# Performance work log

Measured on AMD Instinct MI355X. Metric: run time of the kernel, lower is better.

Reference implementation:

```python
import jax, jax.numpy as jnp
import numpy as np

H = 16
D_NOPE = 128
D_ROPE = 64
D_V = 128
ROPE_BASE = 10000.0
NEG = -1e9


def rotate_half(x):
    h = x.shape[-1] // 2
    return jnp.concatenate([-x[..., h:], x[..., :h]], axis=-1)


def rope_cos_sin(L, dtype=jnp.float32):
    inv_freq = 1.0 / (ROPE_BASE ** (jnp.arange(0, D_ROPE, 2, dtype=jnp.float32) / D_ROPE))
    t = jnp.arange(L, dtype=jnp.float32)
    freqs = jnp.outer(t, inv_freq)                      # (L, D_ROPE/2)
    emb = jnp.concatenate([freqs, freqs], axis=-1)      # (L, D_ROPE)
    return jnp.cos(emb)[None, None].astype(dtype), jnp.sin(emb)[None, None].astype(dtype)


def setup_inputs() -> dict:
    key = jax.random.key(0)
    ks = jax.random.split(key, 8)
    B, L, D = 1, 2048, 2048
    dq, dc = 1536, 512
    dqk = D_NOPE + D_ROPE
    s = 0.02
    hidden_states = jax.random.normal(ks[0], (B, L, D), jnp.float32)
    # causal additive mask, shape (B,1,L,L)
    causal = jnp.tril(jnp.ones((L, L), jnp.bool_))
    attention_mask = jnp.where(causal, 0.0, NEG).astype(jnp.float32)[None, None]
    return {
        "hidden_states": hidden_states,
        "attention_mask": attention_mask,
        "Wq_down": jax.random.normal(ks[1], (D, dq), jnp.float32) * s,
        "Wq_up": jax.random.normal(ks[2], (dq, H * dqk), jnp.float32) * s,
        "Wkv_down": jax.random.normal(ks[3], (D, dc), jnp.float32) * s,
        "Wk_up": jax.random.normal(ks[4], (dc, H * dqk), jnp.float32) * s,
        "Wv_up": jax.random.normal(ks[5], (dc, H * D_V), jnp.float32) * s,
        "Wo": jax.random.normal(ks[6], (H * D_V, D), jnp.float32) * s,
    }


def reference(hidden_states, attention_mask, Wq_down, Wq_up, Wkv_down, Wk_up, Wv_up, Wo):
    B, L, D = hidden_states.shape
    dqk = D_NOPE + D_ROPE
    scale = 1.0 / np.sqrt(dqk).astype(np.float32)

    # low-rank Q path
    q = (hidden_states @ Wq_down) @ Wq_up                       # (B,L,H*dqk)
    q = q.reshape(B, L, H, dqk).transpose(0, 2, 1, 3)           # (B,H,L,dqk)
    # low-rank KV path
    c_kv = hidden_states @ Wkv_down                             # (B,L,dc)
    k = (c_kv @ Wk_up).reshape(B, L, H, dqk).transpose(0, 2, 1, 3)
    v = (c_kv @ Wv_up).reshape(B, L, H, D_V).transpose(0, 2, 1, 3)

    q_nope, q_rope = q[..., :D_NOPE], q[..., D_NOPE:]
    k_nope, k_rope = k[..., :D_NOPE], k[..., D_NOPE:]
    cos, sin = rope_cos_sin(L, hidden_states.dtype)
    q_rope = q_rope * cos + rotate_half(q_rope) * sin
    k_rope = k_rope * cos + rotate_half(k_rope) * sin
    q = jnp.concatenate([q_nope, q_rope], axis=-1)
    k = jnp.concatenate([k_nope, k_rope], axis=-1)

    scores = jnp.einsum("bhqd,bhkd->bhqk", q, k) * scale + attention_mask
    weights = jax.nn.softmax(scores.astype(jnp.float32), axis=-1).astype(q.dtype)
    attn = jnp.einsum("bhqk,bhkd->bhqd", weights, v)            # (B,H,L,D_V)
    attn = attn.transpose(0, 2, 1, 3).reshape(B, L, H * D_V)
    return attn @ Wo
```

## Files before the change

kernel.cpp:

```cpp
#include <hip/hip_runtime.h>
#include <hip/hip_bf16.h>

using bf16 = __hip_bfloat16;
typedef __bf16 bf16x8v __attribute__((ext_vector_type(8)));
typedef float f32x4 __attribute__((ext_vector_type(4)));

static constexpr int SEQ = 2048;
static constexpr int DMODEL = 2048;
static constexpr int NHEADS = 16;
static constexpr int DQKC = 192;
static constexpr int DVC = 128;
static constexpr int DQC = 1536;
static constexpr int DCC = 512;
static constexpr int HQK = NHEADS * DQKC;
static constexpr int HV = NHEADS * DVC;
static constexpr int NKV = HQK + HV;
static constexpr int NDOWN = DQC + DCC;

typedef __attribute__((address_space(1))) const void* gas_ptr;
typedef __attribute__((address_space(3))) void* las_ptr;

__device__ __forceinline__ void g2l16(const void* g, void* l) {
  __builtin_amdgcn_global_load_lds((gas_ptr)g, (las_ptr)l, 16, 0, 0);
}

template <int BM, int BN>
__device__ __forceinline__ void gemm_core(
    const bf16* __restrict__ A, int lda,
    const bf16* __restrict__ Bt, int ldb,
    void* __restrict__ Cv, int ldc,
    int K, float alpha, int c_fp32, long tm, long tn, char* smem)
{
  constexpr int FM = BM / 32, FN = BN / 32;
  bf16* As = (bf16*)smem;
  char* Bsm = smem + BM * 64;
  bf16* Bs = (bf16*)Bsm;
  const int tid = threadIdx.x;
  const int w = tid >> 6, lane = tid & 63;
  const int wm = (w >> 1) * (BM / 2), wn = (w & 1) * (BN / 2);
  const int m0 = lane & 15, q8 = (lane >> 4) * 8;
  f32x4 acc[FM][FN] = {};
  for (int bk = 0; bk < K; bk += 32) {
#pragma unroll
    for (int i = 0; i < BM / 64; i++) {
      const int u = i * 256 + tid;
      g2l16(A + (tm + (u >> 2)) * (long)lda + bk + (u & 3) * 8, smem + u * 16);
    }
#pragma unroll
    for (int i = 0; i < BN / 64; i++) {
      const int u = i * 256 + tid;
      g2l16(Bt + (tn + (u >> 2)) * (long)ldb + bk + (u & 3) * 8, Bsm + u * 16);
    }
    __syncthreads();
    bf16x8v af[FM], bfv[FN];
#pragma unroll
    for (int i = 0; i < FM; i++)
      af[i] = *reinterpret_cast<const bf16x8v*>(&As[(wm + i * 16 + m0) * 32 + q8]);
#pragma unroll
    for (int i = 0; i < FN; i++)
      bfv[i] = *reinterpret_cast<const bf16x8v*>(&Bs[(wn + i * 16 + m0) * 32 + q8]);
#pragma unroll
    for (int mi = 0; mi < FM; mi++)
#pragma unroll
      for (int ni = 0; ni < FN; ni++)
        acc[mi][ni] = __builtin_amdgcn_mfma_f32_16x16x32_bf16(af[mi], bfv[ni], acc[mi][ni], 0, 0, 0);
    __syncthreads();
  }
  const int q4 = (lane >> 4) * 4;
  float* Cf = (float*)Cv;
  bf16* Cb = (bf16*)Cv;
#pragma unroll
  for (int mi = 0; mi < FM; mi++) {
#pragma unroll
    for (int r = 0; r < 4; r++) {
      const long row = tm + wm + mi * 16 + q4 + r;
#pragma unroll
      for (int ni = 0; ni < FN; ni++) {
        const long idx = row * ldc + tn + wn + ni * 16 + m0;
        const float v = acc[mi][ni][r] * alpha;
        if (c_fp32) Cf[idx] = v;
        else Cb[idx] = __float2bfloat16(v);
      }
    }
  }
}

__global__ __launch_bounds__(256) void gemm64(
    const bf16* __restrict__ A, int lda, const bf16* __restrict__ Bt, int ldb,
    void* __restrict__ Cv, int ldc, int K, float alpha, int c_fp32)
{
  __shared__ __align__(16) char smem[(64 + 128) * 64];
  gemm_core<64, 128>(A, lda, Bt, ldb, Cv, ldc, K, alpha, c_fp32,
                     (long)blockIdx.y * 64, (long)blockIdx.x * 128, smem);
}

__global__ __launch_bounds__(256) void gemm_dual(
    const bf16* __restrict__ A1, int lda1, const bf16* __restrict__ B1, int ldb1,
    void* __restrict__ C1, int ldc1, int K1, float alpha1, int nx1,
    const bf16* __restrict__ A2, int lda2, const bf16* __restrict__ B2, int ldb2,
    void* __restrict__ C2, int ldc2, int K2)
{
  __shared__ __align__(16) char smem[(128 + 128) * 64];
  if ((int)blockIdx.x < nx1)
    gemm_core<128, 128>(A1, lda1, B1, ldb1, C1, ldc1, K1, alpha1, 0,
                        (long)blockIdx.y * 128, (long)blockIdx.x * 128, smem);
  else
    gemm_core<128, 128>(A2, lda2, B2, ldb2, C2, ldc2, K2, 1.f, 0,
                        (long)blockIdx.y * 128, (long)((int)blockIdx.x - nx1) * 128, smem);
}

__global__ __launch_bounds__(256) void flash_attn(
    const bf16* __restrict__ qf,
    const bf16* __restrict__ kvf,
    const bf16* __restrict__ vT,
    bf16* __restrict__ attn)
{
  __shared__ __align__(16) char smem[69632];
  const int fid = blockIdx.x;
  const int half = fid >> 8;
  const int r8 = fid & 255;
  const int h = r8 & 15;
  const int t8 = r8 >> 4;
  const int tile = half ? (31 - t8) : t8;
  const int nkt = (tile * 64 + 63) / 96 + 1;
  const int tid = threadIdx.x;
  const int w = tid >> 6, lane = tid & 63;
  const int m0 = lane & 15, quad = lane >> 4;
  const int prow = w * 16 + m0;
  const long qrow = (long)tile * 64 + prow;

  bf16x8v qfr[6];
#pragma unroll
  for (int s = 0; s < 6; s++)
    qfr[s] = *reinterpret_cast<const bf16x8v*>(
        &qf[qrow * HQK + h * DQKC + s * 32 + quad * 8]);

  f32x4 O[8] = {};
  float mrow = -1e30f, lrow = 0.f;

  for (int kt = 0; kt < nkt; ++kt) {
    const int key0 = kt * 96;
#pragma unroll
    for (int i = 0; i < 9; i++) {
      const int u = i * 256 + tid;
      const int key = u / 24;
      const int fg = (u - key * 24) ^ (key & 7);
      g2l16(kvf + (long)(key0 + key) * NKV + h * DQKC + fg * 8, smem + u * 16);
    }
#pragma unroll
    for (int i = 0; i < 8; i++) {
      const int u = i * 256 + tid;
      const int dv = u >> 4;
      const int kg = (u & 15) ^ (dv & 15);
      g2l16(vT + (long)(h * DVC + dv) * SEQ + key0 + kg * 8, smem + 36864 + u * 16);
    }
    __syncthreads();

    f32x4 S[6] = {};
#pragma unroll
    for (int s = 0; s < 6; s++) {
#pragma unroll
      for (int mi = 0; mi < 6; mi++) {
        const int kl = mi * 16 + m0;
        const int idx = kl * 24 + ((s * 4 + quad) ^ (m0 & 7));
        const bf16x8v kb = *reinterpret_cast<const bf16x8v*>(smem + idx * 16);
        S[mi] = __builtin_amdgcn_mfma_f32_16x16x32_bf16(kb, qfr[s], S[mi], 0, 0, 0);
      }
    }
    if (key0 + 95 > tile * 64) {
#pragma unroll
      for (int mi = 0; mi < 6; mi++)
#pragma unroll
        for (int r = 0; r < 4; r++)
          if (key0 + mi * 16 + quad * 4 + r > qrow) S[mi][r] = -1e30f;
    }

    float fm = -1e30f;
#pragma unroll
    for (int mi = 0; mi < 6; mi++)
#pragma unroll
      for (int r = 0; r < 4; r++) fm = fmaxf(fm, S[mi][r]);
    fm = fmaxf(fm, __shfl_xor(fm, 16, 64));
    fm = fmaxf(fm, __shfl_xor(fm, 32, 64));
    const float newm = fmaxf(mrow, fm);
    const float alph = __expf(mrow - newm);
    mrow = newm;
    float ps = 0.f;
#pragma unroll
    for (int mi = 0; mi < 6; mi++)
#pragma unroll
      for (int r = 0; r < 4; r++) {
        const float p = __expf(S[mi][r] - newm);
        S[mi][r] = p;
        ps += p;
      }
    ps += __shfl_xor(ps, 16, 64);
    ps += __shfl_xor(ps, 32, 64);
    lrow = lrow * alph + ps;

    __syncthreads();

#pragma unroll
    for (int mi = 0; mi < 6; mi++) {
      const int k8 = mi * 2 + (quad >> 1);
      const int idx = prow * 16 + (k8 ^ (m0 & 15));
      unsigned short b[4];
#pragma unroll
      for (int r = 0; r < 4; r++) {
        const bf16 t = __float2bfloat16(S[mi][r]);
        b[r] = *reinterpret_cast<const unsigned short*>(&t);
      }
      *reinterpret_cast<uint2*>(smem + idx * 16 + (quad & 1) * 8) =
          make_uint2((unsigned)b[0] | ((unsigned)b[1] << 16),
                     (unsigned)b[2] | ((unsigned)b[3] << 16));
    }
    float aO[4];
#pragma unroll
    for (int r = 0; r < 4; r++) aO[r] = __shfl(alph, quad * 4 + r, 16);
#pragma unroll
    for (int ni = 0; ni < 8; ni++)
#pragma unroll
      for (int r = 0; r < 4; r++) O[ni][r] *= aO[r];

#pragma unroll
    for (int ks = 0; ks < 3; ks++) {
      const int idxp = prow * 16 + ((ks * 4 + quad) ^ (m0 & 15));
      const bf16x8v pa = *reinterpret_cast<const bf16x8v*>(smem + idxp * 16);
#pragma unroll
      for (int ni = 0; ni < 8; ni++) {
        const int dv = ni * 16 + m0;
        const int idxv = dv * 16 + ((ks * 4 + quad) ^ (dv & 15));
        const bf16x8v vb = *reinterpret_cast<const bf16x8v*>(smem + 36864 + idxv * 16);
        O[ni] = __builtin_amdgcn_mfma_f32_16x16x32_bf16(pa, vb, O[ni], 0, 0, 0);
      }
    }
    __syncthreads();
  }

  float lO[4];
#pragma unroll
  for (int r = 0; r < 4; r++) lO[r] = 1.f / __shfl(lrow, quad * 4 + r, 16);
#pragma unroll
  for (int ni = 0; ni < 8; ni++)
#pragma unroll
    for (int r = 0; r < 4; r++)
      attn[((long)tile * 64 + w * 16 + quad * 4 + r) * HV + h * DVC + ni * 16 + m0] =
          __float2bfloat16(O[ni][r] * lO[r]);
}

__device__ __forceinline__ float tofl(float x) { return x; }
__device__ __forceinline__ float tofl(bf16 x) { return __bfloat162float(x); }

template <typename TIN>
__global__ __launch_bounds__(256) void transpose_cast(const TIN* __restrict__ in,
                                                      bf16* __restrict__ out,
                                                      int inStride, int outStride) {
  __shared__ float t[32][33];
  const int bx = blockIdx.x * 32, by = blockIdx.y * 32;
  const int tx = threadIdx.x, ty = threadIdx.y;
#pragma unroll
  for (int j = 0; j < 32; j += 8)
    t[ty + j][tx] = tofl(in[(long)(by + ty + j) * inStride + bx + tx]);
  __syncthreads();
#pragma unroll
  for (int j = 0; j < 32; j += 8)
    out[(long)(bx + ty + j) * outStride + by + tx] = __float2bfloat16(t[tx][ty + j]);
}

struct TPar { const float* src; bf16* dst; int C; int R; int gw; int nblk; };

__global__ __launch_bounds__(256) void transpose6(TPar a, TPar b, TPar c,
                                                  TPar d, TPar e, TPar f) {
  int blk = blockIdx.x;
  TPar p;
  if (blk < a.nblk) p = a;
  else { blk -= a.nblk;
  if (blk < b.nblk) p = b;
  else { blk -= b.nblk;
  if (blk < c.nblk) p = c;
  else { blk -= c.nblk;
  if (blk < d.nblk) p = d;
  else { blk -= d.nblk;
  if (blk < e.nblk) p = e;
  else { blk -= e.nblk; p = f; } } } } }
  const int bx = (blk % p.gw) * 32, by = (blk / p.gw) * 32;
  __shared__ float t[32][33];
  const int tx = threadIdx.x, ty = threadIdx.y;
#pragma unroll
  for (int j = 0; j < 32; j += 8)
    t[ty + j][tx] = p.src[(long)(by + ty + j) * p.C + bx + tx];
  __syncthreads();
#pragma unroll
  for (int j = 0; j < 32; j += 8)
    p.dst[(long)(bx + ty + j) * p.R + by + tx] = __float2bfloat16(t[tx][ty + j]);
}

__global__ __launch_bounds__(256) void cast_f32_bf16(const float* __restrict__ in,
                                                     bf16* __restrict__ out, int n4) {
  int i = blockIdx.x * 256 + threadIdx.x;
  if (i < n4) {
    const float4 v = ((const float4*)in)[i];
    out[i * 4 + 0] = __float2bfloat16(v.x);
    out[i * 4 + 1] = __float2bfloat16(v.y);
    out[i * 4 + 2] = __float2bfloat16(v.z);
    out[i * 4 + 3] = __float2bfloat16(v.w);
  }
}

__global__ __launch_bounds__(256) void rope_qk(bf16* __restrict__ q, bf16* __restrict__ k) {
  const int idx = blockIdx.x * 256 + threadIdx.x;
  const int i = idx & 31;
  const int h = (idx >> 5) & 15;
  const int l = idx >> 9;
  const float inv = powf(10000.f, -(float)i * (1.f / 32.f));
  float s, c;
  sincosf((float)l * inv, &s, &c);
  const long qb = (long)l * HQK + h * DQKC + 128;
  const long kb = (long)l * NKV + h * DQKC + 128;
  {
    float x0 = __bfloat162float(q[qb + i]);
    float x1 = __bfloat162float(q[qb + i + 32]);
    q[qb + i] = __float2bfloat16(x0 * c - x1 * s);
    q[qb + i + 32] = __float2bfloat16(x1 * c + x0 * s);
  }
  {
    float x0 = __bfloat162float(k[kb + i]);
    float x1 = __bfloat162float(k[kb + i + 32]);
    k[kb + i] = __float2bfloat16(x0 * c - x1 * s);
    k[kb + i + 32] = __float2bfloat16(x1 * c + x0 * s);
  }
}

extern "C" void kernel_launch(void* const* d_in, const int* in_sizes, int n_in,
                              void* d_out, int out_size, void* d_ws, size_t ws_size,
                              hipStream_t stream) {
  const float* hs      = (const float*)d_in[0];
  const float* Wq_down = (const float*)d_in[2];
  const float* Wq_up   = (const float*)d_in[3];
  const float* Wkv_down= (const float*)d_in[4];
  const float* Wk_up   = (const float*)d_in[5];
  const float* Wv_up   = (const float*)d_in[6];
  const float* Wo      = (const float*)d_in[7];

  char* p = (char*)d_ws;
  auto alloc = [&](long elems) {
    bf16* r = (bf16*)p;
    p += ((elems * 2 + 255) / 256) * 256;
    return r;
  };
  bf16* hsb   = alloc((long)SEQ * DMODEL);
  bf16* W1T   = alloc((long)NDOWN * DMODEL);
  bf16* WquT  = alloc((long)HQK * DQC);
  bf16* WkvuT = alloc((long)NKV * DCC);
  bf16* WoT   = alloc((long)DMODEL * HV);
  bf16* qdc   = alloc((long)SEQ * NDOWN);
  bf16* qf    = alloc((long)SEQ * HQK);
  bf16* kvf   = alloc((long)SEQ * NKV);
  bf16* vT    = alloc((long)HV * SEQ);
  bf16* attn  = alloc((long)SEQ * HV);

  const float scale = 0.07216878364870323f;

  const dim3 b256(256);
  const dim3 tb(32, 8);
  cast_f32_bf16<<<dim3(SEQ * DMODEL / 4 / 256), b256, 0, stream>>>(hs, hsb, SEQ * DMODEL / 4);

  TPar ta{Wq_down,  W1T,                      DQC,    DMODEL, DQC / 32,    (DQC / 32) * (DMODEL / 32)};
  TPar tb2{Wkv_down, W1T + (long)DQC * DMODEL, DCC,    DMODEL, DCC / 32,    (DCC / 32) * (DMODEL / 32)};
  TPar tc{Wq_up,    WquT,                     HQK,    DQC,    HQK / 32,    (HQK / 32) * (DQC / 32)};
  TPar td{Wk_up,    WkvuT,                    HQK,    DCC,    HQK / 32,    (HQK / 32) * (DCC / 32)};
  TPar te{Wv_up,    WkvuT + (long)HQK * DCC,  HV,     DCC,    HV / 32,     (HV / 32) * (DCC / 32)};
  TPar tf{Wo,       WoT,                      DMODEL, HV,     DMODEL / 32, (DMODEL / 32) * (HV / 32)};
  const int tblk = ta.nblk + tb2.nblk + tc.nblk + td.nblk + te.nblk + tf.nblk;
  transpose6<<<dim3(tblk), tb, 0, stream>>>(ta, tb2, tc, td, te, tf);

  gemm64<<<dim3(NDOWN / 128, SEQ / 64), b256, 0, stream>>>(
      hsb, DMODEL, W1T, DMODEL, qdc, NDOWN, DMODEL, 1.f, 0);

  gemm_dual<<<dim3(HQK / 128 + NKV / 128, SEQ / 128), b256, 0, stream>>>(
      qdc, NDOWN, WquT, DQC, qf, HQK, DQC, scale, HQK / 128,
      qdc + DQC, NDOWN, WkvuT, DCC, kvf, NKV, DCC);

  rope_qk<<<dim3(SEQ * NHEADS * 32 / 256), b256, 0, stream>>>(qf, kvf);
  transpose_cast<bf16><<<dim3(HV / 32, SEQ / 32), tb, 0, stream>>>(kvf + HQK, vT, NKV, SEQ);

  flash_attn<<<dim3(512), b256, 0, stream>>>(qf, kvf, vT, attn);

  gemm64<<<dim3(DMODEL / 128, SEQ / 64), b256, 0, stream>>>(
      attn, HV, WoT, HV, d_out, DMODEL, HV, 1.f, 1);
}
```

Before: 333.6 us.

## Split KV range of long causal attention tiles across two blocks and merge

The upper 16 query tiles, which carry the most causal key blocks, are now split into two blocks that each cover half of the KV range. Each half writes unnormalized fp32 partial outputs plus per-row running max and sum into dead workspace memory. A new combine kernel rescales and merges the two halves into the bf16 output, while the short tiles keep the direct path. The goal is better load balance and more blocks in flight across the CUs, at the cost of extra fp32 partial traffic and one more kernel launch.

```diff
diff --git a/kernel.cpp b/kernel.cpp
--- a/kernel.cpp
+++ b/kernel.cpp
@@ -113,16 +113,31 @@
     const bf16* __restrict__ qf,
     const bf16* __restrict__ kvf,
     const bf16* __restrict__ vT,
-    bf16* __restrict__ attn)
+    bf16* __restrict__ attn,
+    float* __restrict__ Opart,
+    float* __restrict__ Oml)
 {
   __shared__ __align__(16) char smem[69632];
   const int fid = blockIdx.x;
-  const int half = fid >> 8;
-  const int r8 = fid & 255;
-  const int h = r8 & 15;
-  const int t8 = r8 >> 4;
-  const int tile = half ? (31 - t8) : t8;
-  const int nkt = (tile * 64 + 63) / 96 + 1;
+  const int split = fid < 512;
+  int tile, h, ktb, kte, p2;
+  if (split) {
+    tile = 31 - (fid >> 5);
+    h = (fid >> 1) & 15;
+    const int hf = fid & 1;
+    const int nkt = (tile * 64 + 63) / 96 + 1;
+    const int mid = nkt >> 1;
+    ktb = hf ? mid : 0;
+    kte = hf ? nkt : mid;
+    p2 = ((tile - 16) * 16 + h) * 2 + hf;
+  } else {
+    const int f0 = fid - 512;
+    tile = 15 - (f0 >> 4);
+    h = f0 & 15;
+    ktb = 0;
+    kte = (tile * 64 + 63) / 96 + 1;
+    p2 = 0;
+  }
   const int tid = threadIdx.x;
   const int w = tid >> 6, lane = tid & 63;
   const int m0 = lane & 15, quad = lane >> 4;
@@ -138,7 +153,7 @@
   f32x4 O[8] = {};
   float mrow = -1e30f, lrow = 0.f;
 
-  for (int kt = 0; kt < nkt; ++kt) {
+  for (int kt = ktb; kt < kte; ++kt) {
     const int key0 = kt * 96;
 #pragma unroll
     for (int i = 0; i < 9; i++) {
@@ -237,15 +252,58 @@
     __syncthreads();
   }
 
-  float lO[4];
-#pragma unroll
-  for (int r = 0; r < 4; r++) lO[r] = 1.f / __shfl(lrow, quad * 4 + r, 16);
-#pragma unroll
-  for (int ni = 0; ni < 8; ni++)
-#pragma unroll
-    for (int r = 0; r < 4; r++)
-      attn[((long)tile * 64 + w * 16 + quad * 4 + r) * HV + h * DVC + ni * 16 + m0] =
-          __float2bfloat16(O[ni][r] * lO[r]);
+  if (split) {
+    float* Op = Opart + (long)p2 * 64 * 128;
+#pragma unroll
+    for (int ni = 0; ni < 8; ni++)
+#pragma unroll
+      for (int r = 0; r < 4; r++)
+        Op[(w * 16 + quad * 4 + r) * 128 + ni * 16 + m0] = O[ni][r];
+    if (quad == 0) {
+      float* Om = Oml + (long)p2 * 128;
+      Om[(w * 16 + m0) * 2 + 0] = mrow;
+      Om[(w * 16 + m0) * 2 + 1] = lrow;
+    }
+  } else {
+    float lO[4];
+#pragma unroll
+    for (int r = 0; r < 4; r++) lO[r] = 1.f / __shfl(lrow, quad * 4 + r, 16);
+#pragma unroll
+    for (int ni = 0; ni < 8; ni++)
+#pragma unroll
+      for (int r = 0; r < 4; r++)
+        attn[((long)tile * 64 + w * 16 + quad * 4 + r) * HV + h * DVC + ni * 16 + m0] =
+            __float2bfloat16(O[ni][r] * lO[r]);
+  }
+}
+
+__global__ __launch_bounds__(256) void attn_combine(
+    const float* __restrict__ Opart, const float* __restrict__ Oml,
+    bf16* __restrict__ attn)
+{
+  const int p = blockIdx.x;
+  const int tile = 16 + (p >> 4), h = p & 15;
+  const int tid = threadIdx.x;
+  const int row = tid >> 2, dq = tid & 3;
+  const float m0_ = Oml[(p * 2 + 0) * 128 + row * 2];
+  const float l0_ = Oml[(p * 2 + 0) * 128 + row * 2 + 1];
+  const float m1_ = Oml[(p * 2 + 1) * 128 + row * 2];
+  const float l1_ = Oml[(p * 2 + 1) * 128 + row * 2 + 1];
+  const float m = fmaxf(m0_, m1_);
+  const float s0 = __expf(m0_ - m), s1 = __expf(m1_ - m);
+  const float inv = 1.f / (l0_ * s0 + l1_ * s1);
+  const float* O0 = Opart + ((long)(p * 2 + 0) * 64 + row) * 128 + dq * 32;
+  const float* O1 = Opart + ((long)(p * 2 + 1) * 64 + row) * 128 + dq * 32;
+  bf16* out = attn + ((long)tile * 64 + row) * HV + h * DVC + dq * 32;
+#pragma unroll
+  for (int k = 0; k < 32; k += 4) {
+    const float4 a = *reinterpret_cast<const float4*>(O0 + k);
+    const float4 b = *reinterpret_cast<const float4*>(O1 + k);
+    out[k + 0] = __float2bfloat16((a.x * s0 + b.x * s1) * inv);
+    out[k + 1] = __float2bfloat16((a.y * s0 + b.y * s1) * inv);
+    out[k + 2] = __float2bfloat16((a.z * s0 + b.z * s1) * inv);
+    out[k + 3] = __float2bfloat16((a.w * s0 + b.w * s1) * inv);
+  }
 }
 
 __device__ __forceinline__ float tofl(float x) { return x; }
@@ -342,7 +400,8 @@
   const float* Wv_up   = (const float*)d_in[6];
   const float* Wo      = (const float*)d_in[7];
 
-  char* p = (char*)d_ws;
+  char* base = (char*)d_ws;
+  char* p = base;
   auto alloc = [&](long elems) {
     bf16* r = (bf16*)p;
     p += ((elems * 2 + 255) / 256) * 256;
@@ -359,6 +418,9 @@
   bf16* vT    = alloc((long)HV * SEQ);
   bf16* attn  = alloc((long)SEQ * HV);
 
+  float* Opart = (float*)base;
+  float* Oml   = (float*)(base + (long)16 * 1024 * 1024);
+
   const float scale = 0.07216878364870323f;
 
   const dim3 b256(256);
@@ -384,7 +446,8 @@
   rope_qk<<<dim3(SEQ * NHEADS * 32 / 256), b256, 0, stream>>>(qf, kvf);
   transpose_cast<bf16><<<dim3(HV / 32, SEQ / 32), tb, 0, stream>>>(kvf + HQK, vT, NKV, SEQ);
 
-  flash_attn<<<dim3(512), b256, 0, stream>>>(qf, kvf, vT, attn);
+  flash_attn<<<dim3(768), b256, 0, stream>>>(qf, kvf, vT, attn, Opart, Oml);
+  attn_combine<<<dim3(256), b256, 0, stream>>>(Opart, Oml, attn);
 
   gemm64<<<dim3(DMODEL / 128, SEQ / 64), b256, 0, stream>>>(
       attn, HV, WoT, HV, d_out, DMODEL, HV, 1.f, 1);
```

Measured after the change: 368.4 us. +10.5%, slower.

## Double-buffer K/V tiles in flash attention and schedule heaviest query tiles first

Applied to the files above, without the earlier changes.

The flash attention kernel now prefetches the next 96-key K and V^T tiles into a second LDS buffer while computing on the current one. This is meant to hide global-to-LDS load latency behind the MFMA work. The P staging area moves to its own LDS region, which removes the mid-iteration barrier. Blocks are also reordered so the longest causal query tiles launch first, for better load balance. The cost is LDS use rising to about 152 KB per block, which likely allows only one block per CU and so reduces the latency hiding that came from running two blocks at once.

```diff
diff --git a/kernel.cpp b/kernel.cpp
--- a/kernel.cpp
+++ b/kernel.cpp
@@ -109,25 +109,43 @@
                         (long)blockIdx.y * 128, (long)((int)blockIdx.x - nx1) * 128, smem);
 }
 
+__device__ __forceinline__ void fa_stage(
+    const bf16* __restrict__ kvf, const bf16* __restrict__ vT,
+    char* smem, int kbase, int vbase, int key0, int h, int tid)
+{
+#pragma unroll
+  for (int i = 0; i < 9; i++) {
+    const int u = i * 256 + tid;
+    const int key = u / 24;
+    const int fg = (u - key * 24) ^ (key & 7);
+    g2l16(kvf + (long)(key0 + key) * NKV + h * DQKC + fg * 8, smem + kbase + u * 16);
+  }
+#pragma unroll
+  for (int i = 0; i < 8; i++) {
+    const int u = i * 256 + tid;
+    const int dv = u >> 4;
+    const int kg = (u & 15) ^ (dv & 15);
+    g2l16(vT + (long)(h * DVC + dv) * SEQ + key0 + kg * 8, smem + vbase + u * 16);
+  }
+}
+
 __global__ __launch_bounds__(256) void flash_attn(
     const bf16* __restrict__ qf,
     const bf16* __restrict__ kvf,
     const bf16* __restrict__ vT,
     bf16* __restrict__ attn)
 {
-  __shared__ __align__(16) char smem[69632];
+  __shared__ __align__(16) char smem[155648];
   const int fid = blockIdx.x;
-  const int half = fid >> 8;
-  const int r8 = fid & 255;
-  const int h = r8 & 15;
-  const int t8 = r8 >> 4;
-  const int tile = half ? (31 - t8) : t8;
+  const int tile = (fid < 256) ? (31 - (fid >> 4)) : (15 - ((fid - 256) >> 4));
+  const int h = fid & 15;
   const int nkt = (tile * 64 + 63) / 96 + 1;
   const int tid = threadIdx.x;
   const int w = tid >> 6, lane = tid & 63;
   const int m0 = lane & 15, quad = lane >> 4;
   const int prow = w * 16 + m0;
   const long qrow = (long)tile * 64 + prow;
+  constexpr int PSOFF = 139264;
 
   bf16x8v qfr[6];
 #pragma unroll
@@ -138,23 +156,17 @@
   f32x4 O[8] = {};
   float mrow = -1e30f, lrow = 0.f;
 
+  fa_stage(kvf, vT, smem, 0, 73728, 0, h, tid);
+  __syncthreads();
+
   for (int kt = 0; kt < nkt; ++kt) {
+    const int cur = kt & 1;
+    const int kbase = cur * 36864;
+    const int vbase = 73728 + cur * 32768;
     const int key0 = kt * 96;
-#pragma unroll
-    for (int i = 0; i < 9; i++) {
-      const int u = i * 256 + tid;
-      const int key = u / 24;
-      const int fg = (u - key * 24) ^ (key & 7);
-      g2l16(kvf + (long)(key0 + key) * NKV + h * DQKC + fg * 8, smem + u * 16);
-    }
-#pragma unroll
-    for (int i = 0; i < 8; i++) {
-      const int u = i * 256 + tid;
-      const int dv = u >> 4;
-      const int kg = (u & 15) ^ (dv & 15);
-      g2l16(vT + (long)(h * DVC + dv) * SEQ + key0 + kg * 8, smem + 36864 + u * 16);
-    }
-    __syncthreads();
+    if (kt + 1 < nkt)
+      fa_stage(kvf, vT, smem, (cur ^ 1) * 36864, 73728 + (cur ^ 1) * 32768,
+               key0 + 96, h, tid);
 
     f32x4 S[6] = {};
 #pragma unroll
@@ -163,7 +175,7 @@
       for (int mi = 0; mi < 6; mi++) {
         const int kl = mi * 16 + m0;
         const int idx = kl * 24 + ((s * 4 + quad) ^ (m0 & 7));
-        const bf16x8v kb = *reinterpret_cast<const bf16x8v*>(smem + idx * 16);
+        const bf16x8v kb = *reinterpret_cast<const bf16x8v*>(smem + kbase + idx * 16);
         S[mi] = __builtin_amdgcn_mfma_f32_16x16x32_bf16(kb, qfr[s], S[mi], 0, 0, 0);
       }
     }
@@ -198,8 +210,6 @@
     ps += __shfl_xor(ps, 32, 64);
     lrow = lrow * alph + ps;
 
-    __syncthreads();
-
 #pragma unroll
     for (int mi = 0; mi < 6; mi++) {
       const int k8 = mi * 2 + (quad >> 1);
@@ -210,7 +220,7 @@
         const bf16 t = __float2bfloat16(S[mi][r]);
         b[r] = *reinterpret_cast<const unsigned short*>(&t);
       }
-      *reinterpret_cast<uint2*>(smem + idx * 16 + (quad & 1) * 8) =
+      *reinterpret_cast<uint2*>(smem + PSOFF + idx * 16 + (quad & 1) * 8) =
           make_uint2((unsigned)b[0] | ((unsigned)b[1] << 16),
                      (unsigned)b[2] | ((unsigned)b[3] << 16));
     }
@@ -225,12 +235,12 @@
 #pragma unroll
     for (int ks = 0; ks < 3; ks++) {
       const int idxp = prow * 16 + ((ks * 4 + quad) ^ (m0 & 15));
-      const bf16x8v pa = *reinterpret_cast<const bf16x8v*>(smem + idxp * 16);
+      const bf16x8v pa = *reinterpret_cast<const bf16x8v*>(smem + PSOFF + idxp * 16);
 #pragma unroll
       for (int ni = 0; ni < 8; ni++) {
         const int dv = ni * 16 + m0;
         const int idxv = dv * 16 + ((ks * 4 + quad) ^ (dv & 15));
-        const bf16x8v vb = *reinterpret_cast<const bf16x8v*>(smem + 36864 + idxv * 16);
+        const bf16x8v vb = *reinterpret_cast<const bf16x8v*>(smem + vbase + idxv * 16);
         O[ni] = __builtin_amdgcn_mfma_f32_16x16x32_bf16(pa, vb, O[ni], 0, 0, 0);
       }
     }
```

New measurement: 338.5 us. About the same (+1.5%).
